# Kernel tuning notes

Measured on AMD Instinct MI355X. Metric: run time of the kernel, lower is better.

## Reference

```python
import jax, jax.numpy as jnp
import numpy as np

BATCH = 4096
FEATURES = 64
VOCAB = 580000
EMB_DIM = 32
MODELS = 512
SEQ_LEN = 128


def _positional_encoding(position, d_model):
    # Faithful to the numpy get_angles: 1/10000^(2*(i//2)/d_model), sin on even, cos on odd.
    pos = jnp.arange(position, dtype=jnp.float32)[:, None]          # [P, 1]
    i = jnp.arange(d_model, dtype=jnp.float32)[None, :]             # [1, D]
    angle_rates = 1.0 / jnp.power(10000.0, (2.0 * jnp.floor(i / 2.0)) / jnp.float32(d_model))
    angles = pos * angle_rates                                      # [P, D]
    even = (jnp.arange(d_model) % 2 == 0)[None, :]
    pe = jnp.where(even, jnp.sin(angles), jnp.cos(angles))
    return pe[None]                                                 # [1, P, D]


def setup_inputs() -> dict:
    key = jax.random.key(0)
    k1, k2, k3 = jax.random.split(key, 3)
    tokens = jax.random.randint(k1, (BATCH, FEATURES), 0, VOCAB, dtype=jnp.int32)
    emb_table = jax.random.normal(k2, (VOCAB, EMB_DIM), dtype=jnp.float32)
    W = jax.random.normal(k3, (FEATURES * EMB_DIM, MODELS), dtype=jnp.float32) * 0.02
    b = jnp.zeros((MODELS,), dtype=jnp.float32)
    return {"tokens": tokens, "emb_table": emb_table, "W": W, "b": b}


def reference(tokens, emb_table, W, b):
    B, F = tokens.shape
    # gather + scale by sqrt(models)
    x = emb_table[tokens] * jnp.sqrt(jnp.float32(MODELS))           # [B, F, E]
    x = x.reshape(B, F * EMB_DIM)                                   # [B, F*E]
    x = x @ W + b                                                   # [B, M]
    # tf.tile(row, [seq_len]) then reshape (seq_len, models) == broadcast over seq axis
    pe = _positional_encoding(SEQ_LEN, MODELS)                      # [1, S, M]
    out = x[:, None, :] + pe[:, :SEQ_LEN, :]                        # [B, S, M]
    return out
```

## Files before the change

### kernel.cpp

```cpp
#include <hip/hip_runtime.h>
#include <math.h>

#define BATCH   4096
#define FEAT    64
#define EMB     32
#define MODELS  512
#define SEQ     128
#define KDIM    (FEAT * EMB)

#define SQRT_MODELS 22.62741699796952f
#define LN10000     9.210340371976184f

typedef __attribute__((ext_vector_type(4))) float        f32x4;
typedef __attribute__((ext_vector_type(8))) short        bf16x8;
typedef __attribute__((ext_vector_type(4))) unsigned int u32x4;

#define WT_BYTES  ((size_t)MODELS * KDIM * 2)
#define PE_BYTES  ((size_t)SEQ * MODELS * 4)
#define X_BYTES   ((size_t)BATCH * MODELS * 4)
#define ABF_BYTES ((size_t)BATCH * KDIM * 2)
#define WS_MID    (WT_BYTES + PE_BYTES + X_BYTES)
#define WS_FULL   (WT_BYTES + PE_BYTES + X_BYTES + ABF_BYTES)

__device__ inline unsigned short bf16_rne(float f) {
    unsigned int b = __builtin_bit_cast(unsigned int, f);
    return (unsigned short)((b + 0x7FFFu + ((b >> 16) & 1u)) >> 16);
}

#define CVT_PK4(pk, v0, v1)                                                     \
    {                                                                           \
        unsigned int q0, q1, q2, q3;                                            \
        asm("v_cvt_pk_bf16_f32 %0, %1, %2" : "=v"(q0) : "v"(v0.x), "v"(v0.y));  \
        asm("v_cvt_pk_bf16_f32 %0, %1, %2" : "=v"(q1) : "v"(v0.z), "v"(v0.w));  \
        asm("v_cvt_pk_bf16_f32 %0, %1, %2" : "=v"(q2) : "v"(v1.x), "v"(v1.y));  \
        asm("v_cvt_pk_bf16_f32 %0, %1, %2" : "=v"(q3) : "v"(v1.z), "v"(v1.w));  \
        pk = (u32x4){q0, q1, q2, q3};                                           \
    }

__global__ __launch_bounds__(256)
void prep_wt(const float* __restrict__ W, unsigned short* __restrict__ Wt) {
    __shared__ float t[32][33];
    const int k0 = blockIdx.x * 32;
    const int n0 = blockIdx.y * 32;
    const int tx = threadIdx.x;
    const int ty = threadIdx.y;
    #pragma unroll
    for (int i = 0; i < 4; ++i) {
        const int kk = ty + i * 8;
        t[kk][tx] = W[(size_t)(k0 + kk) * MODELS + n0 + tx] * SQRT_MODELS;
    }
    __syncthreads();
    #pragma unroll
    for (int i = 0; i < 4; ++i) {
        const int nn = ty + i * 8;
        Wt[(size_t)(n0 + nn) * KDIM + k0 + tx] = bf16_rne(t[tx][nn]);
    }
}

__global__ __launch_bounds__(256)
void prep_pe(const float* __restrict__ bias, float* __restrict__ pe) {
    const int idx = blockIdx.x * 256 + threadIdx.x;
    const int s = idx >> 9;
    const int m = idx & (MODELS - 1);
    const float rate = expf(-LN10000 * (float)(2 * (m >> 1)) * (1.0f / 512.0f));
    const float ang  = (float)s * rate;
    pe[idx] = ((m & 1) ? cosf(ang) : sinf(ang)) + bias[m];
}

__global__ __launch_bounds__(256)
void gather_a(const int* __restrict__ tokens, const float* __restrict__ emb,
              unsigned short* __restrict__ Abf) {
    const int g    = blockIdx.x * 256 + threadIdx.x;
    const int fr   = g >> 2;
    const int part = g & 3;
    const int tok  = tokens[fr];
    const float* src = emb + (size_t)tok * EMB + part * 8;
    const f32x4 v0 = *(const f32x4*)src;
    const f32x4 v1 = *(const f32x4*)(src + 4);
    u32x4 pk;
    CVT_PK4(pk, v0, v1);
    *(u32x4*)(Abf + (size_t)g * 8) = pk;
}

__global__ __launch_bounds__(256)
void gemm_dense(const unsigned short* __restrict__ Abf,
                const unsigned short* __restrict__ Wt,
                float* __restrict__ x) {
    const int tid  = threadIdx.x;
    const int lane = tid & 63;
    const int wave = tid >> 6;
    const int ln   = lane & 15;
    const int kg   = lane >> 4;
    const int m0 = blockIdx.y * 64 + (wave >> 1) * 32;
    const int n0 = blockIdx.x * 64 + (wave & 1) * 32;

    const unsigned short* a0p = Abf + (size_t)(m0 + ln) * KDIM + kg * 8;
    const unsigned short* a1p = a0p + 16 * KDIM;
    const unsigned short* b0p = Wt + (size_t)(n0 + ln) * KDIM + kg * 8;
    const unsigned short* b1p = b0p + 16 * KDIM;

    f32x4 acc00 = {0,0,0,0}, acc01 = {0,0,0,0};
    f32x4 acc10 = {0,0,0,0}, acc11 = {0,0,0,0};

    #pragma unroll 4
    for (int k = 0; k < KDIM; k += 32) {
        const bf16x8 a0 = *(const bf16x8*)(a0p + k);
        const bf16x8 a1 = *(const bf16x8*)(a1p + k);
        const bf16x8 b0 = *(const bf16x8*)(b0p + k);
        const bf16x8 b1 = *(const bf16x8*)(b1p + k);
        acc00 = __builtin_amdgcn_mfma_f32_16x16x32_bf16(a0, b0, acc00, 0, 0, 0);
        acc01 = __builtin_amdgcn_mfma_f32_16x16x32_bf16(a0, b1, acc01, 0, 0, 0);
        acc10 = __builtin_amdgcn_mfma_f32_16x16x32_bf16(a1, b0, acc10, 0, 0, 0);
        acc11 = __builtin_amdgcn_mfma_f32_16x16x32_bf16(a1, b1, acc11, 0, 0, 0);
    }

    #pragma unroll
    for (int q = 0; q < 4; ++q) {
        const int r = kg * 4 + q;
        x[(size_t)(m0 + r)      * MODELS + n0 + ln]      = acc00[q];
        x[(size_t)(m0 + r)      * MODELS + n0 + 16 + ln] = acc01[q];
        x[(size_t)(m0 + 16 + r) * MODELS + n0 + ln]      = acc10[q];
        x[(size_t)(m0 + 16 + r) * MODELS + n0 + 16 + ln] = acc11[q];
    }
}

__global__ __launch_bounds__(256)
void gemm_mfma(const int* __restrict__ tokens, const float* __restrict__ emb,
               const unsigned short* __restrict__ Wt, float* __restrict__ x) {
    const int tid  = threadIdx.x;
    const int wave = tid >> 6;
    const int lane = tid & 63;
    const int ln   = lane & 15;
    const int kg   = lane >> 4;
    const int m_base = blockIdx.y * 16;
    const int n_base = blockIdx.x * 256 + wave * 64;
    const int* trow = tokens + (size_t)(m_base + ln) * FEAT;
    const unsigned short* bptr[4];
    #pragma unroll
    for (int nf = 0; nf < 4; ++nf)
        bptr[nf] = Wt + (size_t)(n_base + nf * 16 + ln) * KDIM + kg * 8;
    f32x4 acc[4] = {f32x4{0,0,0,0}, f32x4{0,0,0,0}, f32x4{0,0,0,0}, f32x4{0,0,0,0}};
    for (int f4 = 0; f4 < FEAT; f4 += 4) {
        const int4 tok4 = *(const int4*)(trow + f4);
        const int toks[4] = {tok4.x, tok4.y, tok4.z, tok4.w};
        #pragma unroll
        for (int j = 0; j < 4; ++j) {
            const int f = f4 + j;
            const float* ea = emb + (size_t)toks[j] * EMB + kg * 8;
            const f32x4 a0 = *(const f32x4*)ea;
            const f32x4 a1 = *(const f32x4*)(ea + 4);
            u32x4 pk;
            CVT_PK4(pk, a0, a1);
            const bf16x8 afrag = __builtin_bit_cast(bf16x8, pk);
            #pragma unroll
            for (int nf = 0; nf < 4; ++nf) {
                const bf16x8 bfrag = *(const bf16x8*)(bptr[nf] + (size_t)f * EMB);
                acc[nf] = __builtin_amdgcn_mfma_f32_16x16x32_bf16(afrag, bfrag, acc[nf], 0, 0, 0);
            }
        }
    }
    #pragma unroll
    for (int nf = 0; nf < 4; ++nf)
        #pragma unroll
        for (int q = 0; q < 4; ++q)
            x[(size_t)(m_base + kg * 4 + q) * MODELS + n_base + nf * 16 + ln] = acc[nf][q];
}

__global__ __launch_bounds__(256)
void bcast_pe(const float* __restrict__ x, const float* __restrict__ pe,
              float* __restrict__ out) {
    const int tid = threadIdx.x;
    const int m4  = tid & 127;
    const int b   = blockIdx.x * 2 + (tid >> 7);
    const f32x4 xv = *(const f32x4*)(x + (size_t)b * MODELS + m4 * 4);
    const f32x4* pev = (const f32x4*)pe;
    float* ob = out + (size_t)b * SEQ * MODELS + m4 * 4;
    #pragma unroll 4
    for (int s = 0; s < SEQ; ++s) {
        const f32x4 p = pev[s * 128 + m4];
        *(f32x4*)(ob + (size_t)s * MODELS) = xv + p;
    }
}

#define BM 64
#define BN 64
#define BK 32
__global__ __launch_bounds__(256, 2)
void fused_emb_gemm_pe(const int* __restrict__ tokens, const float* __restrict__ emb,
                       const float* __restrict__ W, const float* __restrict__ bias,
                       float* __restrict__ out) {
    __shared__ float As[BK][BM];
    __shared__ float Bs[BK][BN];
    __shared__ float peS[SEQ][BN];
    const int tid  = threadIdx.x;
    const int bn   = blockIdx.x * BN;
    const int brow = blockIdx.y * BM;
    for (int idx = tid; idx < SEQ * BN; idx += 256) {
        const int s  = idx >> 6;
        const int ml = idx & 63;
        const int m  = bn + ml;
        const float rate = expf(-LN10000 * (float)(2 * (m >> 1)) * (1.0f / 512.0f));
        const float ang  = (float)s * rate;
        peS[s][ml] = (m & 1) ? cosf(ang) : sinf(ang);
    }
    float acc[4][4] = {};
    const int tx = tid & 15;
    const int ty = tid >> 4;
    const int lr = tid >> 2;
    const int lj = tid & 3;
    const int bk = tid >> 4;
    const int bc = (tid & 15) * 4;
    for (int kt = 0; kt < FEAT; ++kt) {
        __syncthreads();
        {
            const int tok = tokens[(brow + lr) * FEAT + kt];
            const float* erow = emb + (size_t)tok * EMB + lj * 8;
            const float4 a0 = *(const float4*)(erow);
            const float4 a1 = *(const float4*)(erow + 4);
            const int k0 = lj * 8;
            As[k0 + 0][lr] = a0.x * SQRT_MODELS; As[k0 + 1][lr] = a0.y * SQRT_MODELS;
            As[k0 + 2][lr] = a0.z * SQRT_MODELS; As[k0 + 3][lr] = a0.w * SQRT_MODELS;
            As[k0 + 4][lr] = a1.x * SQRT_MODELS; As[k0 + 5][lr] = a1.y * SQRT_MODELS;
            As[k0 + 6][lr] = a1.z * SQRT_MODELS; As[k0 + 7][lr] = a1.w * SQRT_MODELS;
        }
        {
            const float* w0 = W + (size_t)(kt * 32 + bk) * MODELS + bn + bc;
            const float* w1 = W + (size_t)(kt * 32 + bk + 16) * MODELS + bn + bc;
            *(float4*)&Bs[bk][bc]      = *(const float4*)w0;
            *(float4*)&Bs[bk + 16][bc] = *(const float4*)w1;
        }
        __syncthreads();
        #pragma unroll
        for (int k = 0; k < BK; ++k) {
            const float4 a = *(const float4*)&As[k][ty * 4];
            const float4 b = *(const float4*)&Bs[k][tx * 4];
            acc[0][0] += a.x * b.x; acc[0][1] += a.x * b.y; acc[0][2] += a.x * b.z; acc[0][3] += a.x * b.w;
            acc[1][0] += a.y * b.x; acc[1][1] += a.y * b.y; acc[1][2] += a.y * b.z; acc[1][3] += a.y * b.w;
            acc[2][0] += a.z * b.x; acc[2][1] += a.z * b.y; acc[2][2] += a.z * b.z; acc[2][3] += a.z * b.w;
            acc[3][0] += a.w * b.x; acc[3][1] += a.w * b.y; acc[3][2] += a.w * b.z; acc[3][3] += a.w * b.w;
        }
    }
    {
        const float4 bv = *(const float4*)(bias + bn + tx * 4);
        #pragma unroll
        for (int i = 0; i < 4; ++i) {
            acc[i][0] += bv.x; acc[i][1] += bv.y; acc[i][2] += bv.z; acc[i][3] += bv.w;
        }
    }
    size_t rowbase[4];
    #pragma unroll
    for (int i = 0; i < 4; ++i)
        rowbase[i] = ((size_t)(brow + ty * 4 + i) * SEQ) * MODELS + bn + tx * 4;
    #pragma unroll 4
    for (int s = 0; s < SEQ; ++s) {
        const float4 pv = *(const float4*)&peS[s][tx * 4];
        const size_t soff = (size_t)s * MODELS;
        #pragma unroll
        for (int i = 0; i < 4; ++i) {
            float4 o;
            o.x = acc[i][0] + pv.x; o.y = acc[i][1] + pv.y;
            o.z = acc[i][2] + pv.z; o.w = acc[i][3] + pv.w;
            *(float4*)(out + rowbase[i] + soff) = o;
        }
    }
}

extern "C" void kernel_launch(void* const* d_in, const int* in_sizes, int n_in,
                              void* d_out, int out_size, void* d_ws, size_t ws_size,
                              hipStream_t stream) {
    const int*   tokens = (const int*)d_in[0];
    const float* emb    = (const float*)d_in[1];
    const float* W      = (const float*)d_in[2];
    const float* bias   = (const float*)d_in[3];
    float*       out    = (float*)d_out;

    if (ws_size >= WS_FULL) {
        char* w = (char*)d_ws;
        unsigned short* Wt  = (unsigned short*)w;
        float*          pe  = (float*)(w + WT_BYTES);
        float*          x   = (float*)(w + WT_BYTES + PE_BYTES);
        unsigned short* Abf = (unsigned short*)(w + WT_BYTES + PE_BYTES + X_BYTES);

        prep_wt<<<dim3(KDIM / 32, MODELS / 32), dim3(32, 8), 0, stream>>>(W, Wt);
        prep_pe<<<dim3(SEQ * MODELS / 256), dim3(256), 0, stream>>>(bias, pe);
        gather_a<<<dim3(BATCH * KDIM / 8 / 256), dim3(256), 0, stream>>>(tokens, emb, Abf);
        gemm_dense<<<dim3(MODELS / 64, BATCH / 64), dim3(256), 0, stream>>>(Abf, Wt, x);
        bcast_pe<<<dim3(BATCH / 2), dim3(256), 0, stream>>>(x, pe, out);
    } else if (ws_size >= WS_MID) {
        char* w = (char*)d_ws;
        unsigned short* Wt = (unsigned short*)w;
        float* pe = (float*)(w + WT_BYTES);
        float* x  = (float*)(w + WT_BYTES + PE_BYTES);

        prep_wt<<<dim3(KDIM / 32, MODELS / 32), dim3(32, 8), 0, stream>>>(W, Wt);
        prep_pe<<<dim3(SEQ * MODELS / 256), dim3(256), 0, stream>>>(bias, pe);
        gemm_mfma<<<dim3(MODELS / 256, BATCH / 16), dim3(256), 0, stream>>>(tokens, emb, Wt, x);
        bcast_pe<<<dim3(BATCH / 2), dim3(256), 0, stream>>>(x, pe, out);
    } else {
        fused_emb_gemm_pe<<<dim3(MODELS / BN, BATCH / BM), dim3(256), 0, stream>>>(
            tokens, emb, W, bias, out);
    }
}
```

Before: 278.2 us.

## Fuse pipeline into one cooperative kernel overlapping GEMM half with output writes

Replaces the five-kernel sequence (weight transpose, PE table, gather, GEMM, broadcast) with a single cooperative persistent kernel of 768 blocks that uses grid-wide syncs between phases. The GEMM is split into two batch halves so that while 256 blocks compute the second half, the remaining blocks stream the broadcast+PE output for the first half. The aim is to remove launch gaps and hide the output write traffic behind matrix compute. The cost is grid.sync overhead, a fixed grid that must fit co-resident, and a GEMM using only 256 blocks with no LDS reuse. The mid-workspace path is dropped and a fallback to the multi-kernel path is kept.

```diff
diff --git a/kernel.cpp b/kernel.cpp
--- a/kernel.cpp
+++ b/kernel.cpp
@@ -1,5 +1,8 @@
 #include <hip/hip_runtime.h>
+#include <hip/hip_cooperative_groups.h>
 #include <math.h>
+
+namespace cg = cooperative_groups;
 
 #define BATCH   4096
 #define FEAT    64
@@ -21,6 +24,9 @@
 #define ABF_BYTES ((size_t)BATCH * KDIM * 2)
 #define WS_MID    (WT_BYTES + PE_BYTES + X_BYTES)
 #define WS_FULL   (WT_BYTES + PE_BYTES + X_BYTES + ABF_BYTES)
+
+#define NBLK   768
+#define CHUNK  2048
 
 __device__ inline unsigned short bf16_rne(float f) {
     unsigned int b = __builtin_bit_cast(unsigned int, f);
@@ -37,6 +43,121 @@
         pk = (u32x4){q0, q1, q2, q3};                                           \
     }
 
+__device__ inline void gemm_tilegroup(int g, int base,
+                                      const unsigned short* __restrict__ Abf,
+                                      const unsigned short* __restrict__ Wt,
+                                      float* __restrict__ x, int tid) {
+    const int wave = tid >> 6;
+    const int lane = tid & 63;
+    const int ln   = lane & 15;
+    const int kg   = lane >> 4;
+    const int t  = g * 4 + wave;
+    const int m0 = base + (t >> 3) * 16;
+    const int n0 = (t & 7) * 64;
+
+    const unsigned short* ap = Abf + (size_t)(m0 + ln) * KDIM + kg * 8;
+    const unsigned short* bp = Wt  + (size_t)(n0 + ln) * KDIM + kg * 8;
+
+    f32x4 acc[4] = {f32x4{0,0,0,0}, f32x4{0,0,0,0}, f32x4{0,0,0,0}, f32x4{0,0,0,0}};
+
+    #pragma unroll 4
+    for (int k = 0; k < KDIM; k += 32) {
+        const bf16x8 a = *(const bf16x8*)(ap + k);
+        #pragma unroll
+        for (int nf = 0; nf < 4; ++nf) {
+            const bf16x8 b = *(const bf16x8*)(bp + (size_t)nf * 16 * KDIM + k);
+            acc[nf] = __builtin_amdgcn_mfma_f32_16x16x32_bf16(a, b, acc[nf], 0, 0, 0);
+        }
+    }
+    #pragma unroll
+    for (int nf = 0; nf < 4; ++nf)
+        #pragma unroll
+        for (int q = 0; q < 4; ++q)
+            x[(size_t)(m0 + kg * 4 + q) * MODELS + n0 + nf * 16 + ln] = acc[nf][q];
+}
+
+__device__ inline void write_row_span(const float* __restrict__ x, const float* __restrict__ pe,
+                                      float* __restrict__ out, int row, int s0, int ns, int tid) {
+    const int col = (tid & 127) * 4;
+    const int sl  = tid >> 7;
+    const f32x4 xv = *(const f32x4*)(x + (size_t)row * MODELS + col);
+    float* ob = out + (size_t)row * SEQ * MODELS + col;
+    for (int s = s0 + sl; s < s0 + ns; s += 2)
+        *(f32x4*)(ob + (size_t)s * MODELS) = xv + *(const f32x4*)(pe + (size_t)s * MODELS + col);
+}
+
+__global__ __launch_bounds__(256, 4)
+void coop_all(const int* __restrict__ tokens, const float* __restrict__ emb,
+              const float* __restrict__ W, const float* __restrict__ bias,
+              unsigned short* __restrict__ Wt, float* __restrict__ pe,
+              unsigned short* __restrict__ Abf, float* __restrict__ x,
+              float* __restrict__ out) {
+    cg::grid_group grid = cg::this_grid();
+    const int bid = blockIdx.x;
+    const int tid = threadIdx.x;
+
+    __shared__ float t[32][33];
+
+    {
+        const int tx = tid & 31, ty = tid >> 5;
+        #pragma unroll 1
+        for (int rep = 0; rep < 2; ++rep) {
+            const int T = bid + rep * NBLK;
+            if (T < 1024) {
+                const int k0 = (T & 63) * 32, n0 = (T >> 6) * 32;
+                #pragma unroll
+                for (int i = 0; i < 4; ++i)
+                    t[ty + i * 8][tx] = W[(size_t)(k0 + ty + i * 8) * MODELS + n0 + tx] * SQRT_MODELS;
+                __syncthreads();
+                #pragma unroll
+                for (int i = 0; i < 4; ++i)
+                    Wt[(size_t)(n0 + ty + i * 8) * KDIM + k0 + tx] = bf16_rne(t[tx][ty + i * 8]);
+                __syncthreads();
+            }
+        }
+    }
+    if (bid >= 256 && bid < 512) {
+        const int idx = (bid - 256) * 256 + tid;
+        const int s = idx >> 9, m = idx & (MODELS - 1);
+        const float rate = expf(-LN10000 * (float)(2 * (m >> 1)) * (1.0f / 512.0f));
+        const float ang  = (float)s * rate;
+        pe[idx] = ((m & 1) ? cosf(ang) : sinf(ang)) + bias[m];
+    }
+    for (int u = bid * 256 + tid; u < BATCH * FEAT * 4; u += NBLK * 256) {
+        const int tok = tokens[u >> 2];
+        const float* src = emb + (size_t)tok * EMB + (u & 3) * 8;
+        const f32x4 v0 = *(const f32x4*)src;
+        const f32x4 v1 = *(const f32x4*)(src + 4);
+        u32x4 pk;
+        CVT_PK4(pk, v0, v1);
+        *(u32x4*)(Abf + (size_t)u * 8) = pk;
+    }
+
+    grid.sync();
+
+    if (bid < 256) gemm_tilegroup(bid, 0, Abf, Wt, x, tid);
+
+    grid.sync();
+
+    if (bid < 256) {
+        gemm_tilegroup(bid, CHUNK, Abf, Wt, x, tid);
+    } else {
+        const int wid = bid - 256;
+        #pragma unroll 1
+        for (int r = 0; r < 4; ++r)
+            write_row_span(x, pe, out, wid * 4 + r, 0, SEQ, tid);
+    }
+
+    grid.sync();
+
+    #pragma unroll 1
+    for (int u = bid; u < CHUNK * 4; u += NBLK) {
+        const int row = CHUNK + (u >> 2);
+        const int q   = u & 3;
+        write_row_span(x, pe, out, row, q * 32, 32, tid);
+    }
+}
+
 __global__ __launch_bounds__(256)
 void prep_wt(const float* __restrict__ W, unsigned short* __restrict__ Wt) {
     __shared__ float t[32][33];
@@ -45,16 +166,12 @@
     const int tx = threadIdx.x;
     const int ty = threadIdx.y;
     #pragma unroll
-    for (int i = 0; i < 4; ++i) {
-        const int kk = ty + i * 8;
-        t[kk][tx] = W[(size_t)(k0 + kk) * MODELS + n0 + tx] * SQRT_MODELS;
-    }
+    for (int i = 0; i < 4; ++i)
+        t[ty + i * 8][tx] = W[(size_t)(k0 + ty + i * 8) * MODELS + n0 + tx] * SQRT_MODELS;
     __syncthreads();
     #pragma unroll
-    for (int i = 0; i < 4; ++i) {
-        const int nn = ty + i * 8;
-        Wt[(size_t)(n0 + nn) * KDIM + k0 + tx] = bf16_rne(t[tx][nn]);
-    }
+    for (int i = 0; i < 4; ++i)
+        Wt[(size_t)(n0 + ty + i * 8) * KDIM + k0 + tx] = bf16_rne(t[tx][ty + i * 8]);
 }
 
 __global__ __launch_bounds__(256)
@@ -113,7 +230,6 @@
         acc10 = __builtin_amdgcn_mfma_f32_16x16x32_bf16(a1, b0, acc10, 0, 0, 0);
         acc11 = __builtin_amdgcn_mfma_f32_16x16x32_bf16(a1, b1, acc11, 0, 0, 0);
     }
-
     #pragma unroll
     for (int q = 0; q < 4; ++q) {
         const int r = kg * 4 + q;
@@ -122,48 +238,6 @@
         x[(size_t)(m0 + 16 + r) * MODELS + n0 + ln]      = acc10[q];
         x[(size_t)(m0 + 16 + r) * MODELS + n0 + 16 + ln] = acc11[q];
     }
-}
-
-__global__ __launch_bounds__(256)
-void gemm_mfma(const int* __restrict__ tokens, const float* __restrict__ emb,
-               const unsigned short* __restrict__ Wt, float* __restrict__ x) {
-    const int tid  = threadIdx.x;
-    const int wave = tid >> 6;
-    const int lane = tid & 63;
-    const int ln   = lane & 15;
-    const int kg   = lane >> 4;
-    const int m_base = blockIdx.y * 16;
-    const int n_base = blockIdx.x * 256 + wave * 64;
-    const int* trow = tokens + (size_t)(m_base + ln) * FEAT;
-    const unsigned short* bptr[4];
-    #pragma unroll
-    for (int nf = 0; nf < 4; ++nf)
-        bptr[nf] = Wt + (size_t)(n_base + nf * 16 + ln) * KDIM + kg * 8;
-    f32x4 acc[4] = {f32x4{0,0,0,0}, f32x4{0,0,0,0}, f32x4{0,0,0,0}, f32x4{0,0,0,0}};
-    for (int f4 = 0; f4 < FEAT; f4 += 4) {
-        const int4 tok4 = *(const int4*)(trow + f4);
-        const int toks[4] = {tok4.x, tok4.y, tok4.z, tok4.w};
-        #pragma unroll
-        for (int j = 0; j < 4; ++j) {
-            const int f = f4 + j;
-            const float* ea = emb + (size_t)toks[j] * EMB + kg * 8;
-            const f32x4 a0 = *(const f32x4*)ea;
-            const f32x4 a1 = *(const f32x4*)(ea + 4);
-            u32x4 pk;
-            CVT_PK4(pk, a0, a1);
-            const bf16x8 afrag = __builtin_bit_cast(bf16x8, pk);
-            #pragma unroll
-            for (int nf = 0; nf < 4; ++nf) {
-                const bf16x8 bfrag = *(const bf16x8*)(bptr[nf] + (size_t)f * EMB);
-                acc[nf] = __builtin_amdgcn_mfma_f32_16x16x32_bf16(afrag, bfrag, acc[nf], 0, 0, 0);
-            }
-        }
-    }
-    #pragma unroll
-    for (int nf = 0; nf < 4; ++nf)
-        #pragma unroll
-        for (int q = 0; q < 4; ++q)
-            x[(size_t)(m_base + kg * 4 + q) * MODELS + n_base + nf * 16 + ln] = acc[nf][q];
 }
 
 __global__ __launch_bounds__(256)
@@ -265,6 +339,19 @@
     }
 }
 
+static void launch_r4(const int* tokens, const float* emb, const float* W,
+                      const float* bias, float* out, char* w, hipStream_t stream) {
+    unsigned short* Wt  = (unsigned short*)w;
+    float*          pe  = (float*)(w + WT_BYTES);
+    float*          x   = (float*)(w + WT_BYTES + PE_BYTES);
+    unsigned short* Abf = (unsigned short*)(w + WT_BYTES + PE_BYTES + X_BYTES);
+    prep_wt<<<dim3(KDIM / 32, MODELS / 32), dim3(32, 8), 0, stream>>>(W, Wt);
+    prep_pe<<<dim3(SEQ * MODELS / 256), dim3(256), 0, stream>>>(bias, pe);
+    gather_a<<<dim3(BATCH * KDIM / 8 / 256), dim3(256), 0, stream>>>(tokens, emb, Abf);
+    gemm_dense<<<dim3(MODELS / 64, BATCH / 64), dim3(256), 0, stream>>>(Abf, Wt, x);
+    bcast_pe<<<dim3(BATCH / 2), dim3(256), 0, stream>>>(x, pe, out);
+}
+
 extern "C" void kernel_launch(void* const* d_in, const int* in_sizes, int n_in,
                               void* d_out, int out_size, void* d_ws, size_t ws_size,
                               hipStream_t stream) {
@@ -281,21 +368,22 @@
         float*          x   = (float*)(w + WT_BYTES + PE_BYTES);
         unsigned short* Abf = (unsigned short*)(w + WT_BYTES + PE_BYTES + X_BYTES);
 
-        prep_wt<<<dim3(KDIM / 32, MODELS / 32), dim3(32, 8), 0, stream>>>(W, Wt);
-        prep_pe<<<dim3(SEQ * MODELS / 256), dim3(256), 0, stream>>>(bias, pe);
-        gather_a<<<dim3(BATCH * KDIM / 8 / 256), dim3(256), 0, stream>>>(tokens, emb, Abf);
-        gemm_dense<<<dim3(MODELS / 64, BATCH / 64), dim3(256), 0, stream>>>(Abf, Wt, x);
-        bcast_pe<<<dim3(BATCH / 2), dim3(256), 0, stream>>>(x, pe, out);
-    } else if (ws_size >= WS_MID) {
-        char* w = (char*)d_ws;
-        unsigned short* Wt = (unsigned short*)w;
-        float* pe = (float*)(w + WT_BYTES);
-        float* x  = (float*)(w + WT_BYTES + PE_BYTES);
-
-        prep_wt<<<dim3(KDIM / 32, MODELS / 32), dim3(32, 8), 0, stream>>>(W, Wt);
-        prep_pe<<<dim3(SEQ * MODELS / 256), dim3(256), 0, stream>>>(bias, pe);
-        gemm_mfma<<<dim3(MODELS / 256, BATCH / 16), dim3(256), 0, stream>>>(tokens, emb, Wt, x);
-        bcast_pe<<<dim3(BATCH / 2), dim3(256), 0, stream>>>(x, pe, out);
+        int dev = 0, coop = 0;
+        hipGetDevice(&dev);
+        hipDeviceGetAttribute(&coop, hipDeviceAttributeCooperativeLaunch, dev);
+
+        if (coop) {
+            void* args[] = {(void*)&tokens, (void*)&emb, (void*)&W, (void*)&bias,
+                            (void*)&Wt, (void*)&pe, (void*)&Abf, (void*)&x, (void*)&out};
+            hipError_t e = hipLaunchCooperativeKernel((const void*)coop_all, dim3(NBLK),
+                                                      dim3(256), args, 0, stream);
+            if (e != hipSuccess) {
+                (void)hipGetLastError();
+                launch_r4(tokens, emb, W, bias, out, w, stream);
+            }
+        } else {
+            launch_r4(tokens, emb, W, bias, out, w, stream);
+        }
     } else {
         fused_emb_gemm_pe<<<dim3(MODELS / BN, BATCH / BM), dim3(256), 0, stream>>>(
             tokens, emb, W, bias, out);
```

After: 565.6 us. 103% more time.
